# Optimization experiments

Measured on AMD Instinct MI355X. Metric: run time of the kernel, lower is better.

Reference implementation:

```python
import jax, jax.numpy as jnp
import numpy as np

D = 1024
H = 8
K = 6
TEMP = 0.1
LN_EPS = 1e-5


def _ln(x, g, b):
    m = jnp.mean(x, axis=-1, keepdims=True)
    v = jnp.mean((x - m) ** 2, axis=-1, keepdims=True)
    return (x - m) / jnp.sqrt(v + LN_EPS) * g + b


def setup_inputs() -> dict:
    key = jax.random.key(0)
    ks = jax.random.split(key, 8)
    B, T = 8, 4096
    s = 0.02
    inp = {
        'video_features': jax.random.normal(ks[0], (B, T, D), jnp.float32),
        'query_embedding': jax.random.normal(ks[1], (B, D), jnp.float32),
        'mu_w1': jax.random.normal(ks[2], (D, D), jnp.float32) * s,
        'mu_b1': jnp.zeros((D,), jnp.float32),
        'mu_g': jnp.ones((D,), jnp.float32),
        'mu_be': jnp.zeros((D,), jnp.float32),
        'mu_w2': jax.random.normal(ks[3], (D, D), jnp.float32) * s,
        'mu_b2': jnp.zeros((D,), jnp.float32),
        'sg_w1': jax.random.normal(ks[4], (D, D), jnp.float32) * s,
        'sg_b1': jnp.zeros((D,), jnp.float32),
        'sg_g': jnp.ones((D,), jnp.float32),
        'sg_be': jnp.zeros((D,), jnp.float32),
        'sg_w2': jax.random.normal(ks[5], (D, D), jnp.float32) * s,
        'sg_b2': jnp.zeros((D,), jnp.float32),
        'in_w': jax.random.normal(ks[6], (3 * D, D), jnp.float32) * s,
        'in_b': jnp.zeros((3 * D,), jnp.float32),
        'out_w': jax.random.normal(ks[7], (D, D), jnp.float32) * s,
        'out_b': jnp.zeros((D,), jnp.float32),
    }
    return inp


def reference(video_features, query_embedding, mu_w1, mu_b1, mu_g, mu_be, mu_w2, mu_b2,
              sg_w1, sg_b1, sg_g, sg_be, sg_w2, sg_b2, in_w, in_b, out_w, out_b):
    B, T, _ = video_features.shape
    dh = D // H

    # mu / sigma estimators (Linear -> LN -> ReLU -> Linear [-> Softplus])
    mu_q = jax.nn.relu(_ln(query_embedding @ mu_w1.T + mu_b1, mu_g, mu_be)) @ mu_w2.T + mu_b2  # [B,D]
    sigma_q = jax.nn.softplus(
        jax.nn.relu(_ln(query_embedding @ sg_w1.T + sg_b1, sg_g, sg_be)) @ sg_w2.T + sg_b2) + 1e-6

    # Mahalanobis (diagonal) distances [B,T]
    centered = video_features - mu_q[:, None, :]
    dist = jnp.sum(centered ** 2 / sigma_q[:, None, :], axis=-1)

    # distance weights around the (torch lower) median
    med = jnp.sort(dist, axis=1)[:, (T - 1) // 2][:, None]
    dist_w = jnp.exp(-jnp.abs(dist - med) / TEMP)  # [B,T]

    # single-query multihead attention (torch MHA, averaged attn weights)
    wq, wk, wv = in_w[:D], in_w[D:2 * D], in_w[2 * D:]
    bq, bk, bv = in_b[:D], in_b[D:2 * D], in_b[2 * D:]
    q = (mu_q @ wq.T + bq).reshape(B, H, dh)                  # [B,H,dh]
    k = (video_features @ wk.T + bk).reshape(B, T, H, dh)     # [B,T,H,dh]
    scores = jnp.einsum('bhd,bthd->bht', q, k) / jnp.sqrt(jnp.asarray(dh, q.dtype))
    attn = jax.nn.softmax(scores, axis=-1)                    # [B,H,T]
    attn_w = jnp.mean(attn, axis=1)                           # [B,T] head-averaged

    combined = dist_w * attn_w  # [B,T]

    # greedy diverse top-k (farthest-point style), vectorized over batch
    ar = jnp.arange(T)
    idx0 = jnp.argmax(combined, axis=1)                       # [B]
    sel_mask = ar[None, :] == idx0[:, None]
    min_d = jnp.abs(ar[None, :] - idx0[:, None]).astype(combined.dtype)
    picks = [idx0]
    for _ in range(K - 1):
        score = jnp.where(sel_mask, -jnp.inf, min_d * combined)
        nxt = jnp.argmax(score, axis=1)
        picks.append(nxt)
        sel_mask = sel_mask | (ar[None, :] == nxt[:, None])
        min_d = jnp.minimum(min_d, jnp.abs(ar[None, :] - nxt[:, None]).astype(combined.dtype))
    indices = jnp.stack(picks, axis=1)  # [B,K]

    rep = jnp.take_along_axis(video_features, indices[:, :, None], axis=1)  # [B,K,D]

    # NTLBG loss
    rep_dist = jnp.take_along_axis(dist, indices, axis=1)  # [B,K]
    target = jnp.sort(rep_dist, axis=1)[:, (K - 1) // 2][:, None]
    ellipsoid = jnp.mean((rep_dist - target) ** 2)
    centered_rep = rep - mu_q[:, None, :]
    consistency = jnp.mean(jnp.sum(centered_rep ** 2 / sigma_q[:, None, :], axis=-1))
    sim = jnp.einsum('bkd,bjd->bkj', rep, rep)
    tri = jnp.triu(jnp.ones((K, K), rep.dtype), k=1)
    diversity = jnp.mean((sim * tri) ** 2)
    loss = ellipsoid + 0.1 * consistency + 0.05 * diversity

    return rep, indices, combined, dist, mu_q, sigma_q, loss
```

## Files before the change

kernel.cpp:

```cpp
#include <hip/hip_runtime.h>
#include <math.h>

#define BD   8
#define TT   4096
#define DD   1024
#define HH   8
#define KK   6
#define OFF_REP   0
#define OFF_IDX   49152
#define OFF_COMB  49200
#define OFF_DIST  81968
#define OFF_MU    114736
#define OFF_SG    122928
#define OFF_LOSS  131120
#define WS_X1     0
#define WS_H      16384
#define WS_Q      32768
#define WS_P      40960
#define WS_C      106496
#define WS_ISIG   106560
#define WS_SCORES 114752

#define INV_SQRT_DH 0.08838834764831845f

__device__ __forceinline__ float softplus_f(float x) {
  return fmaxf(x, 0.0f) + log1pf(expf(-fabsf(x)));
}

__device__ __forceinline__ void gemv_rows_core(const float* __restrict__ in,
                                               const float* __restrict__ W,
                                               int row, float (*s_in)[DD], float acc[8]) {
  int tid = threadIdx.x;
  const float4* in4 = (const float4*)in;
  float4* s4 = (float4*)&s_in[0][0];
  for (int i = tid; i < 2048; i += 256) s4[i] = in4[i];
  __syncthreads();
  int lane = tid & 63;
  const float4* wr4 = (const float4*)(W + (size_t)row * DD);
#pragma unroll
  for (int b = 0; b < 8; ++b) acc[b] = 0.0f;
#pragma unroll
  for (int i = 0; i < 4; ++i) {
    int d4 = i * 64 + lane;
    float4 w4 = wr4[d4];
#pragma unroll
    for (int b = 0; b < 8; ++b) {
      float4 q4 = ((const float4*)&s_in[b][0])[d4];
      acc[b] += w4.x * q4.x + w4.y * q4.y + w4.z * q4.z + w4.w * q4.w;
    }
  }
#pragma unroll
  for (int off = 32; off; off >>= 1)
#pragma unroll
    for (int b = 0; b < 8; ++b) acc[b] += __shfl_xor(acc[b], off, 64);
}

__global__ __launch_bounds__(256) void k_gemv_pre(const float* __restrict__ qe,
    const float* __restrict__ W0, const float* __restrict__ W1,
    const float* __restrict__ b0, const float* __restrict__ b1, float* __restrict__ x1) {
  __shared__ float s_in[8][DD];
  int path = blockIdx.x >> 8;
  int row = (blockIdx.x & 255) * 4 + (threadIdx.x >> 6);
  const float* W = path ? W1 : W0;
  const float* bb = path ? b1 : b0;
  float acc[8];
  gemv_rows_core(qe, W, row, s_in, acc);
  if ((threadIdx.x & 63) == 0) {
    float bv = bb[row];
#pragma unroll
    for (int b = 0; b < 8; ++b) x1[path * 8192 + b * DD + row] = acc[b] + bv;
  }
}

__global__ __launch_bounds__(256) void k_ln(const float* __restrict__ x1,
    const float* __restrict__ g0, const float* __restrict__ be0,
    const float* __restrict__ g1, const float* __restrict__ be1, float* __restrict__ h) {
  int path = blockIdx.x >> 3, b = blockIdx.x & 7;
  const float* x = x1 + path * 8192 + b * DD;
  const float* g = path ? g1 : g0;
  const float* be = path ? be1 : be0;
  __shared__ float sx[DD];
  __shared__ float red[256];
  int tid = threadIdx.x;
  float ps = 0.0f;
  for (int i = tid; i < DD; i += 256) { float v = x[i]; sx[i] = v; ps += v; }
  red[tid] = ps; __syncthreads();
  for (int off = 128; off; off >>= 1) { if (tid < off) red[tid] += red[tid + off]; __syncthreads(); }
  float mean = red[0] * (1.0f / 1024.0f);
  __syncthreads();
  float pv = 0.0f;
  for (int i = tid; i < DD; i += 256) { float d = sx[i] - mean; pv += d * d; }
  red[tid] = pv; __syncthreads();
  for (int off = 128; off; off >>= 1) { if (tid < off) red[tid] += red[tid + off]; __syncthreads(); }
  float var = red[0] * (1.0f / 1024.0f);
  float inv = 1.0f / sqrtf(var + 1e-5f);
  for (int i = tid; i < DD; i += 256) {
    float v = (sx[i] - mean) * inv * g[i] + be[i];
    h[path * 8192 + b * DD + i] = v > 0.0f ? v : 0.0f;
  }
}

__global__ __launch_bounds__(256) void k_gemv_mid(const float* __restrict__ h,
    const float* __restrict__ W0, const float* __restrict__ W1,
    const float* __restrict__ b0, const float* __restrict__ b1,
    float* __restrict__ mu_out, float* __restrict__ sg_out, float* __restrict__ isig) {
  __shared__ float s_in[8][DD];
  int path = blockIdx.x >> 8;
  int row = (blockIdx.x & 255) * 4 + (threadIdx.x >> 6);
  const float* W = path ? W1 : W0;
  const float* bb = path ? b1 : b0;
  float acc[8];
  gemv_rows_core(h + path * 8192, W, row, s_in, acc);
  if ((threadIdx.x & 63) == 0) {
    float bv = bb[row];
#pragma unroll
    for (int b = 0; b < 8; ++b) {
      float v = acc[b] + bv;
      if (path == 0) {
        mu_out[b * DD + row] = v;
      } else {
        float sp = softplus_f(v) + 1e-6f;
        sg_out[b * DD + row] = sp;
        isig[b * DD + row] = 1.0f / sp;
      }
    }
  }
}

__global__ __launch_bounds__(256) void k_gemv_q(const float* __restrict__ mu_q,
    const float* __restrict__ in_w, const float* __restrict__ in_b, float* __restrict__ q) {
  __shared__ float s_in[8][DD];
  int row = blockIdx.x * 4 + (threadIdx.x >> 6);
  float acc[8];
  gemv_rows_core(mu_q, in_w, row, s_in, acc);
  if ((threadIdx.x & 63) == 0) {
    float bv = in_b[row];
#pragma unroll
    for (int b = 0; b < 8; ++b) q[b * DD + row] = acc[b] + bv;
  }
}

__global__ __launch_bounds__(256) void k_p(const float* __restrict__ q,
    const float* __restrict__ in_w, const float* __restrict__ in_b,
    float* __restrict__ p, float* __restrict__ c) {
  int hh = blockIdx.x >> 2;
  int j0 = (blockIdx.x & 3) * 256;
  __shared__ float qh[8][128];
  for (int i = threadIdx.x; i < 1024; i += 256) {
    int b = i >> 7, r = i & 127;
    qh[b][r] = q[b * DD + hh * 128 + r];
  }
  __syncthreads();
  const float* wbase = in_w + (size_t)(DD + hh * 128) * DD + j0 + threadIdx.x;
  float acc[8];
#pragma unroll
  for (int b = 0; b < 8; ++b) acc[b] = 0.0f;
  for (int r = 0; r < 128; ++r) {
    float w = wbase[(size_t)r * DD];
#pragma unroll
    for (int b = 0; b < 8; ++b) acc[b] += qh[b][r] * w;
  }
#pragma unroll
  for (int b = 0; b < 8; ++b) p[(b * HH + hh) * DD + j0 + threadIdx.x] = acc[b] * INV_SQRT_DH;
  if ((blockIdx.x & 3) == 0 && threadIdx.x < 8) {
    int b = threadIdx.x;
    float cc = 0.0f;
    for (int r = 0; r < 128; ++r) cc += qh[b][r] * in_b[DD + hh * 128 + r];
    c[b * HH + hh] = cc * INV_SQRT_DH;
  }
}

__global__ __launch_bounds__(256, 4) void k_main(const float* __restrict__ video,
    const float* __restrict__ mu_q, const float* __restrict__ isig,
    const float* __restrict__ p, const float* __restrict__ c,
    float* __restrict__ dist_out, float* __restrict__ scores, float* __restrict__ loss_out) {
  __shared__ float s_mu[DD];
  __shared__ float s_is[DD];
  __shared__ float s_p[HH][DD];
  int b = blockIdx.x >> 8;
  int chunk = blockIdx.x & 255;
  int tid = threadIdx.x;
  int wave = tid >> 6, lane = tid & 63;
  if (blockIdx.x == 0 && tid == 0) loss_out[0] = 0.0f;
  float4* s_mu4 = (float4*)s_mu;
  float4* s_is4 = (float4*)s_is;
  float4* s_p4 = (float4*)&s_p[0][0];
  s_mu4[tid] = ((const float4*)(mu_q + b * DD))[tid];
  s_is4[tid] = ((const float4*)(isig + b * DD))[tid];
  const float4* pg4 = (const float4*)(p + b * HH * DD);
  for (int i = tid; i < 2048; i += 256) s_p4[i] = pg4[i];
  __syncthreads();

  int t0 = chunk * 16 + wave * 4;
  const float4* v4 = (const float4*)(video + ((size_t)(b * TT + t0)) * DD);
  double dacc[4] = {0.0, 0.0, 0.0, 0.0};
  float sacc[4][8];
#pragma unroll
  for (int t = 0; t < 4; ++t)
#pragma unroll
    for (int hh = 0; hh < 8; ++hh) sacc[t][hh] = 0.0f;

#pragma unroll 2
  for (int i = 0; i < 4; ++i) {
    int d4 = i * 64 + lane;
    float4 vv0 = v4[0 * 256 + d4];
    float4 vv1 = v4[1 * 256 + d4];
    float4 vv2 = v4[2 * 256 + d4];
    float4 vv3 = v4[3 * 256 + d4];
    {
      float4 mu4 = s_mu4[d4];
      float4 is4 = s_is4[d4];
      float dx, dy, dz, dw, e;
      dx = vv0.x - mu4.x; dy = vv0.y - mu4.y; dz = vv0.z - mu4.z; dw = vv0.w - mu4.w;
      e = dx * dx * is4.x + dy * dy * is4.y + dz * dz * is4.z + dw * dw * is4.w;
      dacc[0] += (double)e;
      dx = vv1.x - mu4.x; dy = vv1.y - mu4.y; dz = vv1.z - mu4.z; dw = vv1.w - mu4.w;
      e = dx * dx * is4.x + dy * dy * is4.y + dz * dz * is4.z + dw * dw * is4.w;
      dacc[1] += (double)e;
      dx = vv2.x - mu4.x; dy = vv2.y - mu4.y; dz = vv2.z - mu4.z; dw = vv2.w - mu4.w;
      e = dx * dx * is4.x + dy * dy * is4.y + dz * dz * is4.z + dw * dw * is4.w;
      dacc[2] += (double)e;
      dx = vv3.x - mu4.x; dy = vv3.y - mu4.y; dz = vv3.z - mu4.z; dw = vv3.w - mu4.w;
      e = dx * dx * is4.x + dy * dy * is4.y + dz * dz * is4.z + dw * dw * is4.w;
      dacc[3] += (double)e;
    }
#pragma unroll
    for (int hh = 0; hh < 8; ++hh) {
      float4 pp = ((const float4*)&s_p[hh][0])[d4];
      sacc[0][hh] += pp.x * vv0.x + pp.y * vv0.y + pp.z * vv0.z + pp.w * vv0.w;
      sacc[1][hh] += pp.x * vv1.x + pp.y * vv1.y + pp.z * vv1.z + pp.w * vv1.w;
      sacc[2][hh] += pp.x * vv2.x + pp.y * vv2.y + pp.z * vv2.z + pp.w * vv2.w;
      sacc[3][hh] += pp.x * vv3.x + pp.y * vv3.y + pp.z * vv3.z + pp.w * vv3.w;
    }
  }
#pragma unroll
  for (int off = 32; off; off >>= 1) {
#pragma unroll
    for (int t = 0; t < 4; ++t) {
      dacc[t] += __shfl_xor(dacc[t], off, 64);
#pragma unroll
      for (int hh = 0; hh < 8; ++hh) sacc[t][hh] += __shfl_xor(sacc[t][hh], off, 64);
    }
  }
  if (lane < 4) {
    int t = lane;
    int tt = t0 + t;
    dist_out[b * TT + tt] = (float)dacc[t];
#pragma unroll
    for (int hh = 0; hh < 8; ++hh)
      scores[(size_t)(b * HH + hh) * TT + tt] = sacc[t][hh] + c[b * HH + hh];
  }
}

__global__ __launch_bounds__(1024) void k_epilogue(const float* __restrict__ scores,
    const float* __restrict__ dist, const float* __restrict__ video,
    float* __restrict__ comb_out, float* __restrict__ idx_out,
    float* __restrict__ rep, float* __restrict__ loss_out) {
  int b = blockIdx.x;
  int tid = threadIdx.x;
  int wave = tid >> 6, lane = tid & 63;
  __shared__ float s_dist[TT];
  __shared__ float s_hm[HH], s_hs[HH];
  __shared__ float s_w16[16], s_w16b[16];
  __shared__ unsigned hist[256];
  __shared__ unsigned wsum[4];
  __shared__ unsigned s_sel;
  __shared__ int s_kk;
  __shared__ float wv[16];
  __shared__ int wi[16];
  __shared__ int s_pick;
  __shared__ float wdiv[16];
  __shared__ float repb[KK * DD];

  {
    int h = tid >> 7, lt = tid & 127;
    const float4* srow4 = (const float4*)(scores + ((size_t)(b * HH + h)) * TT);
    float m = -INFINITY;
#pragma unroll
    for (int i = 0; i < 8; ++i) {
      float4 v = srow4[lt + i * 128];
      m = fmaxf(m, fmaxf(fmaxf(v.x, v.y), fmaxf(v.z, v.w)));
    }
#pragma unroll
    for (int off = 32; off; off >>= 1) m = fmaxf(m, __shfl_xor(m, off, 64));
    if (lane == 0) s_w16[wave] = m;
    __syncthreads();
    float mh = fmaxf(s_w16[h * 2], s_w16[h * 2 + 1]);
    float s = 0.0f;
#pragma unroll
    for (int i = 0; i < 8; ++i) {
      float4 v = srow4[lt + i * 128];
      s += expf(v.x - mh) + expf(v.y - mh) + expf(v.z - mh) + expf(v.w - mh);
    }
#pragma unroll
    for (int off = 32; off; off >>= 1) s += __shfl_xor(s, off, 64);
    if (lane == 0) s_w16b[wave] = s;
    __syncthreads();
    if (lt == 0) { s_hm[h] = mh; s_hs[h] = 1.0f / (s_w16b[h * 2] + s_w16b[h * 2 + 1]); }
    __syncthreads();
  }

  float4 d4 = ((const float4*)(dist + b * TT))[tid];
  ((float4*)s_dist)[tid] = d4;
  float4 aw = make_float4(0.f, 0.f, 0.f, 0.f);
#pragma unroll
  for (int h = 0; h < HH; ++h) {
    float4 sc = ((const float4*)(scores + ((size_t)(b * HH + h)) * TT))[tid];
    float mh = s_hm[h], is = s_hs[h];
    aw.x += expf(sc.x - mh) * is;
    aw.y += expf(sc.y - mh) * is;
    aw.z += expf(sc.z - mh) * is;
    aw.w += expf(sc.w - mh) * is;
  }
  aw.x *= 0.125f; aw.y *= 0.125f; aw.z *= 0.125f; aw.w *= 0.125f;
  uint4 keys;
  keys.x = __float_as_uint(d4.x);
  keys.y = __float_as_uint(d4.y);
  keys.z = __float_as_uint(d4.z);
  keys.w = __float_as_uint(d4.w);
  __syncthreads();

  unsigned prefix = 0;
  int kk = (TT - 1) / 2;
  for (int pass = 0; pass < 4; ++pass) {
    int shift = 24 - 8 * pass;
    if (tid < 256) hist[tid] = 0;
    __syncthreads();
    {
      unsigned karr[4] = {keys.x, keys.y, keys.z, keys.w};
#pragma unroll
      for (int j = 0; j < 4; ++j) {
        unsigned key = karr[j];
        bool ok = (pass == 0) || ((key >> (shift + 8)) == prefix);
        if (ok) atomicAdd(&hist[(key >> shift) & 255], 1u);
      }
    }
    __syncthreads();
    unsigned hcnt = 0, inc = 0;
    if (tid < 256) {
      hcnt = hist[tid];
      inc = hcnt;
#pragma unroll
      for (int off = 1; off < 64; off <<= 1) {
        unsigned v = __shfl_up(inc, off, 64);
        if (lane >= off) inc += v;
      }
      if (lane == 63) wsum[wave] = inc;
    }
    __syncthreads();
    if (tid < 256) {
      unsigned base = 0;
      for (int w = 0; w < wave; ++w) base += wsum[w];
      unsigned excl = base + inc - hcnt;
      if ((int)excl <= kk && kk < (int)(excl + hcnt)) {
        s_sel = (prefix << 8) | (unsigned)tid;
        s_kk = kk - (int)excl;
      }
    }
    __syncthreads();
    prefix = s_sel;
    kk = s_kk;
    __syncthreads();
  }
  float med = __uint_as_float(prefix);

  float4 cb;
  cb.x = expf(-fabsf(d4.x - med) / 0.1f) * aw.x;
  cb.y = expf(-fabsf(d4.y - med) / 0.1f) * aw.y;
  cb.z = expf(-fabsf(d4.z - med) / 0.1f) * aw.z;
  cb.w = expf(-fabsf(d4.w - med) / 0.1f) * aw.w;
  ((float4*)(comb_out + b * TT))[tid] = cb;

  float4 md = make_float4(0.f, 0.f, 0.f, 0.f);
  int i0 = tid * 4;
  int picks[KK];
  for (int k = 0; k < KK; ++k) {
    float carr[4] = {cb.x, cb.y, cb.z, cb.w};
    float marr[4] = {md.x, md.y, md.z, md.w};
    float best = -INFINITY; int bi = 1 << 30;
#pragma unroll
    for (int j = 0; j < 4; ++j) {
      float cv = carr[j];
      float sc = (k == 0) ? cv : ((cv < 0.0f) ? -INFINITY : marr[j] * cv);
      if (sc > best) { best = sc; bi = i0 + j; }
    }
#pragma unroll
    for (int off = 32; off; off >>= 1) {
      float ov = __shfl_xor(best, off, 64);
      int oi = __shfl_xor(bi, off, 64);
      if (ov > best || (ov == best && oi < bi)) { best = ov; bi = oi; }
    }
    if (lane == 0) { wv[wave] = best; wi[wave] = bi; }
    __syncthreads();
    if (tid == 0) {
      float bb2 = wv[0]; int ii = wi[0];
#pragma unroll
      for (int w = 1; w < 16; ++w)
        if (wv[w] > bb2 || (wv[w] == bb2 && wi[w] < ii)) { bb2 = wv[w]; ii = wi[w]; }
      s_pick = ii;
    }
    __syncthreads();
    int pick = s_pick;
    picks[k] = pick;
    if ((pick >> 2) == tid) {
      int j = pick & 3;
      if (j == 0) cb.x = -1.0f; else if (j == 1) cb.y = -1.0f;
      else if (j == 2) cb.z = -1.0f; else cb.w = -1.0f;
    }
    float dn0 = fabsf((float)(i0 + 0 - pick));
    float dn1 = fabsf((float)(i0 + 1 - pick));
    float dn2 = fabsf((float)(i0 + 2 - pick));
    float dn3 = fabsf((float)(i0 + 3 - pick));
    if (k == 0) { md.x = dn0; md.y = dn1; md.z = dn2; md.w = dn3; }
    else { md.x = fminf(md.x, dn0); md.y = fminf(md.y, dn1);
           md.z = fminf(md.z, dn2); md.w = fminf(md.w, dn3); }
  }
  if (tid < KK) idx_out[b * KK + tid] = (float)picks[tid];

  float4* repb4 = (float4*)repb;
  float4* rep4 = (float4*)(rep + (size_t)b * KK * DD);
  for (int e = tid; e < KK * (DD / 4); e += 1024) {
    int k = e >> 8, dd4 = e & 255;
    const float4* vrow = (const float4*)(video + ((size_t)(b * TT + picks[k])) * DD);
    float4 v = vrow[dd4];
    rep4[(size_t)k * (DD / 4) + dd4] = v;
    repb4[e] = v;
  }
  __syncthreads();

  const int pk[15] = {0,0,0,0,0,1,1,1,1,2,2,2,3,3,4};
  const int pj[15] = {1,2,3,4,5,2,3,4,5,3,4,5,4,5,5};
  float divacc = 0.0f;
  if (wave < 15) {
    int a = pk[wave], j = pj[wave];
    float part = 0.0f;
    for (int d = lane; d < DD; d += 64) part += repb[a * DD + d] * repb[j * DD + d];
#pragma unroll
    for (int off = 32; off; off >>= 1) part += __shfl_xor(part, off, 64);
    if (lane == 0) divacc = part * part;
  }
  if (lane == 0) wdiv[wave] = (wave < 15) ? divacc : 0.0f;
  __syncthreads();

  if (tid == 0) {
    float div = 0.0f;
#pragma unroll
    for (int w = 0; w < 15; ++w) div += wdiv[w];
    float rd[KK], srt[KK];
#pragma unroll
    for (int k = 0; k < KK; ++k) { rd[k] = s_dist[picks[k]]; srt[k] = rd[k]; }
    for (int a = 1; a < KK; ++a) {
      float key = srt[a]; int b2 = a - 1;
      while (b2 >= 0 && srt[b2] > key) { srt[b2 + 1] = srt[b2]; --b2; }
      srt[b2 + 1] = key;
    }
    float target = srt[(KK - 1) / 2];
    float ell = 0.0f, cons = 0.0f;
#pragma unroll
    for (int k = 0; k < KK; ++k) { float d = rd[k] - target; ell += d * d; cons += rd[k]; }
    float partial = ell * (1.0f / 48.0f) + 0.1f * cons * (1.0f / 48.0f) + 0.05f * div * (1.0f / 288.0f);
    atomicAdd(loss_out, partial);
  }
}

extern "C" void kernel_launch(void* const* d_in, const int* in_sizes, int n_in,
                              void* d_out, int out_size, void* d_ws, size_t ws_size,
                              hipStream_t stream) {
  const float* video = (const float*)d_in[0];
  const float* qe    = (const float*)d_in[1];
  const float* mu_w1 = (const float*)d_in[2];
  const float* mu_b1 = (const float*)d_in[3];
  const float* mu_g  = (const float*)d_in[4];
  const float* mu_be = (const float*)d_in[5];
  const float* mu_w2 = (const float*)d_in[6];
  const float* mu_b2 = (const float*)d_in[7];
  const float* sg_w1 = (const float*)d_in[8];
  const float* sg_b1 = (const float*)d_in[9];
  const float* sg_g  = (const float*)d_in[10];
  const float* sg_be = (const float*)d_in[11];
  const float* sg_w2 = (const float*)d_in[12];
  const float* sg_b2 = (const float*)d_in[13];
  const float* in_w  = (const float*)d_in[14];
  const float* in_b  = (const float*)d_in[15];
  float* out = (float*)d_out;
  float* ws  = (float*)d_ws;

  k_gemv_pre<<<512, 256, 0, stream>>>(qe, mu_w1, sg_w1, mu_b1, sg_b1, ws + WS_X1);
  k_ln<<<16, 256, 0, stream>>>(ws + WS_X1, mu_g, mu_be, sg_g, sg_be, ws + WS_H);
  k_gemv_mid<<<512, 256, 0, stream>>>(ws + WS_H, mu_w2, sg_w2, mu_b2, sg_b2,
                                      out + OFF_MU, out + OFF_SG, ws + WS_ISIG);
  k_gemv_q<<<256, 256, 0, stream>>>(out + OFF_MU, in_w, in_b, ws + WS_Q);
  k_p<<<32, 256, 0, stream>>>(ws + WS_Q, in_w, in_b, ws + WS_P, ws + WS_C);
  k_main<<<2048, 256, 0, stream>>>(video, out + OFF_MU, ws + WS_ISIG, ws + WS_P, ws + WS_C,
                                   out + OFF_DIST, ws + WS_SCORES, out + OFF_LOSS);
  k_epilogue<<<8, 1024, 0, stream>>>(ws + WS_SCORES, out + OFF_DIST, video,
                                     out + OFF_COMB, out + OFF_IDX, out + OFF_REP, out + OFF_LOSS);
}
```

Baseline: 332.2 us.

## Fuse softmax exp and sums into main kernel, privatize radix histogram

The main kernel now exponentiates the attention scores without max subtraction and accumulates per-head sums with shared then global atomics. The epilogue therefore only normalises instead of running separate max and sum passes over the scores. The per-batch query-bias constant c is dropped, since it cancels in the softmax. LayerNorm is rewritten as a single-pass float4 kernel with wave shuffles, and the median radix select uses per-wave private histograms to reduce atomic contention. Risks: exp overflow without a max shift, nondeterministic atomic sums, and less accurate single-pass variance.

```diff
diff --git a/kernel.cpp b/kernel.cpp
--- a/kernel.cpp
+++ b/kernel.cpp
@@ -17,9 +17,9 @@
 #define WS_H      16384
 #define WS_Q      32768
 #define WS_P      40960
-#define WS_C      106496
+#define WS_SUMS   106496
 #define WS_ISIG   106560
-#define WS_SCORES 114752
+#define WS_ES     114752
 
 #define INV_SQRT_DH 0.08838834764831845f
 
@@ -76,28 +76,32 @@
     const float* __restrict__ g0, const float* __restrict__ be0,
     const float* __restrict__ g1, const float* __restrict__ be1, float* __restrict__ h) {
   int path = blockIdx.x >> 3, b = blockIdx.x & 7;
-  const float* x = x1 + path * 8192 + b * DD;
-  const float* g = path ? g1 : g0;
-  const float* be = path ? be1 : be0;
-  __shared__ float sx[DD];
-  __shared__ float red[256];
-  int tid = threadIdx.x;
-  float ps = 0.0f;
-  for (int i = tid; i < DD; i += 256) { float v = x[i]; sx[i] = v; ps += v; }
-  red[tid] = ps; __syncthreads();
-  for (int off = 128; off; off >>= 1) { if (tid < off) red[tid] += red[tid + off]; __syncthreads(); }
-  float mean = red[0] * (1.0f / 1024.0f);
-  __syncthreads();
-  float pv = 0.0f;
-  for (int i = tid; i < DD; i += 256) { float d = sx[i] - mean; pv += d * d; }
-  red[tid] = pv; __syncthreads();
-  for (int off = 128; off; off >>= 1) { if (tid < off) red[tid] += red[tid + off]; __syncthreads(); }
-  float var = red[0] * (1.0f / 1024.0f);
+  const float4* x4 = (const float4*)(x1 + path * 8192 + b * DD);
+  const float4* g4 = (const float4*)(path ? g1 : g0);
+  const float4* be4 = (const float4*)(path ? be1 : be0);
+  int tid = threadIdx.x, wave = tid >> 6, lane = tid & 63;
+  __shared__ float ws1[4], ws2[4];
+  float4 v = x4[tid];
+  float s = v.x + v.y + v.z + v.w;
+  float s2 = v.x * v.x + v.y * v.y + v.z * v.z + v.w * v.w;
+#pragma unroll
+  for (int off = 32; off; off >>= 1) {
+    s += __shfl_xor(s, off, 64);
+    s2 += __shfl_xor(s2, off, 64);
+  }
+  if (lane == 0) { ws1[wave] = s; ws2[wave] = s2; }
+  __syncthreads();
+  s = ws1[0] + ws1[1] + ws1[2] + ws1[3];
+  s2 = ws2[0] + ws2[1] + ws2[2] + ws2[3];
+  float mean = s * (1.0f / 1024.0f);
+  float var = s2 * (1.0f / 1024.0f) - mean * mean;
   float inv = 1.0f / sqrtf(var + 1e-5f);
-  for (int i = tid; i < DD; i += 256) {
-    float v = (sx[i] - mean) * inv * g[i] + be[i];
-    h[path * 8192 + b * DD + i] = v > 0.0f ? v : 0.0f;
-  }
+  float4 g = g4[tid], be = be4[tid], o;
+  o.x = fmaxf((v.x - mean) * inv * g.x + be.x, 0.0f);
+  o.y = fmaxf((v.y - mean) * inv * g.y + be.y, 0.0f);
+  o.z = fmaxf((v.z - mean) * inv * g.z + be.z, 0.0f);
+  o.w = fmaxf((v.w - mean) * inv * g.w + be.w, 0.0f);
+  ((float4*)(h + path * 8192 + b * DD))[tid] = o;
 }
 
 __global__ __launch_bounds__(256) void k_gemv_mid(const float* __restrict__ h,
@@ -141,8 +145,12 @@
 }
 
 __global__ __launch_bounds__(256) void k_p(const float* __restrict__ q,
-    const float* __restrict__ in_w, const float* __restrict__ in_b,
-    float* __restrict__ p, float* __restrict__ c) {
+    const float* __restrict__ in_w, float* __restrict__ p,
+    float* __restrict__ sums, float* __restrict__ loss_out) {
+  if (blockIdx.x == 0) {
+    if (threadIdx.x < 64) sums[threadIdx.x] = 0.0f;
+    else if (threadIdx.x == 64) loss_out[0] = 0.0f;
+  }
   int hh = blockIdx.x >> 2;
   int j0 = (blockIdx.x & 3) * 256;
   __shared__ float qh[8][128];
@@ -162,26 +170,20 @@
   }
 #pragma unroll
   for (int b = 0; b < 8; ++b) p[(b * HH + hh) * DD + j0 + threadIdx.x] = acc[b] * INV_SQRT_DH;
-  if ((blockIdx.x & 3) == 0 && threadIdx.x < 8) {
-    int b = threadIdx.x;
-    float cc = 0.0f;
-    for (int r = 0; r < 128; ++r) cc += qh[b][r] * in_b[DD + hh * 128 + r];
-    c[b * HH + hh] = cc * INV_SQRT_DH;
-  }
 }
 
 __global__ __launch_bounds__(256, 4) void k_main(const float* __restrict__ video,
     const float* __restrict__ mu_q, const float* __restrict__ isig,
-    const float* __restrict__ p, const float* __restrict__ c,
-    float* __restrict__ dist_out, float* __restrict__ scores, float* __restrict__ loss_out) {
+    const float* __restrict__ p,
+    float* __restrict__ dist_out, float* __restrict__ es, float* __restrict__ sums) {
   __shared__ float s_mu[DD];
   __shared__ float s_is[DD];
   __shared__ float s_p[HH][DD];
+  __shared__ float s_esum[HH];
   int b = blockIdx.x >> 8;
   int chunk = blockIdx.x & 255;
   int tid = threadIdx.x;
   int wave = tid >> 6, lane = tid & 63;
-  if (blockIdx.x == 0 && tid == 0) loss_out[0] = 0.0f;
   float4* s_mu4 = (float4*)s_mu;
   float4* s_is4 = (float4*)s_is;
   float4* s_p4 = (float4*)&s_p[0][0];
@@ -189,6 +191,7 @@
   s_is4[tid] = ((const float4*)(isig + b * DD))[tid];
   const float4* pg4 = (const float4*)(p + b * HH * DD);
   for (int i = tid; i < 2048; i += 256) s_p4[i] = pg4[i];
+  if (tid < HH) s_esum[tid] = 0.0f;
   __syncthreads();
 
   int t0 = chunk * 16 + wave * 4;
@@ -247,12 +250,18 @@
     int tt = t0 + t;
     dist_out[b * TT + tt] = (float)dacc[t];
 #pragma unroll
-    for (int hh = 0; hh < 8; ++hh)
-      scores[(size_t)(b * HH + hh) * TT + tt] = sacc[t][hh] + c[b * HH + hh];
-  }
-}
-
-__global__ __launch_bounds__(1024) void k_epilogue(const float* __restrict__ scores,
+    for (int hh = 0; hh < 8; ++hh) {
+      float ev = expf(sacc[t][hh]);
+      es[(size_t)(b * HH + hh) * TT + tt] = ev;
+      atomicAdd(&s_esum[hh], ev);
+    }
+  }
+  __syncthreads();
+  if (tid < HH) atomicAdd(&sums[b * HH + tid], s_esum[tid]);
+}
+
+__global__ __launch_bounds__(1024) void k_epilogue(const float* __restrict__ es,
+    const float* __restrict__ sums,
     const float* __restrict__ dist, const float* __restrict__ video,
     float* __restrict__ comb_out, float* __restrict__ idx_out,
     float* __restrict__ rep, float* __restrict__ loss_out) {
@@ -260,9 +269,8 @@
   int tid = threadIdx.x;
   int wave = tid >> 6, lane = tid & 63;
   __shared__ float s_dist[TT];
-  __shared__ float s_hm[HH], s_hs[HH];
-  __shared__ float s_w16[16], s_w16b[16];
-  __shared__ unsigned hist[256];
+  __shared__ float s_hs[HH];
+  __shared__ unsigned whist[16][256];
   __shared__ unsigned wsum[4];
   __shared__ unsigned s_sel;
   __shared__ int s_kk;
@@ -272,45 +280,20 @@
   __shared__ float wdiv[16];
   __shared__ float repb[KK * DD];
 
-  {
-    int h = tid >> 7, lt = tid & 127;
-    const float4* srow4 = (const float4*)(scores + ((size_t)(b * HH + h)) * TT);
-    float m = -INFINITY;
-#pragma unroll
-    for (int i = 0; i < 8; ++i) {
-      float4 v = srow4[lt + i * 128];
-      m = fmaxf(m, fmaxf(fmaxf(v.x, v.y), fmaxf(v.z, v.w)));
-    }
-#pragma unroll
-    for (int off = 32; off; off >>= 1) m = fmaxf(m, __shfl_xor(m, off, 64));
-    if (lane == 0) s_w16[wave] = m;
-    __syncthreads();
-    float mh = fmaxf(s_w16[h * 2], s_w16[h * 2 + 1]);
-    float s = 0.0f;
-#pragma unroll
-    for (int i = 0; i < 8; ++i) {
-      float4 v = srow4[lt + i * 128];
-      s += expf(v.x - mh) + expf(v.y - mh) + expf(v.z - mh) + expf(v.w - mh);
-    }
-#pragma unroll
-    for (int off = 32; off; off >>= 1) s += __shfl_xor(s, off, 64);
-    if (lane == 0) s_w16b[wave] = s;
-    __syncthreads();
-    if (lt == 0) { s_hm[h] = mh; s_hs[h] = 1.0f / (s_w16b[h * 2] + s_w16b[h * 2 + 1]); }
-    __syncthreads();
-  }
+  if (tid < HH) s_hs[tid] = 1.0f / sums[b * HH + tid];
+  __syncthreads();
 
   float4 d4 = ((const float4*)(dist + b * TT))[tid];
   ((float4*)s_dist)[tid] = d4;
   float4 aw = make_float4(0.f, 0.f, 0.f, 0.f);
 #pragma unroll
   for (int h = 0; h < HH; ++h) {
-    float4 sc = ((const float4*)(scores + ((size_t)(b * HH + h)) * TT))[tid];
-    float mh = s_hm[h], is = s_hs[h];
-    aw.x += expf(sc.x - mh) * is;
-    aw.y += expf(sc.y - mh) * is;
-    aw.z += expf(sc.z - mh) * is;
-    aw.w += expf(sc.w - mh) * is;
+    float4 e4 = ((const float4*)(es + ((size_t)(b * HH + h)) * TT))[tid];
+    float is = s_hs[h];
+    aw.x += e4.x * is;
+    aw.y += e4.y * is;
+    aw.z += e4.z * is;
+    aw.w += e4.w * is;
   }
   aw.x *= 0.125f; aw.y *= 0.125f; aw.z *= 0.125f; aw.w *= 0.125f;
   uint4 keys;
@@ -318,13 +301,12 @@
   keys.y = __float_as_uint(d4.y);
   keys.z = __float_as_uint(d4.z);
   keys.w = __float_as_uint(d4.w);
-  __syncthreads();
 
   unsigned prefix = 0;
   int kk = (TT - 1) / 2;
   for (int pass = 0; pass < 4; ++pass) {
     int shift = 24 - 8 * pass;
-    if (tid < 256) hist[tid] = 0;
+    ((uint4*)whist)[tid] = make_uint4(0u, 0u, 0u, 0u);
     __syncthreads();
     {
       unsigned karr[4] = {keys.x, keys.y, keys.z, keys.w};
@@ -332,13 +314,14 @@
       for (int j = 0; j < 4; ++j) {
         unsigned key = karr[j];
         bool ok = (pass == 0) || ((key >> (shift + 8)) == prefix);
-        if (ok) atomicAdd(&hist[(key >> shift) & 255], 1u);
+        if (ok) atomicAdd(&whist[wave][(key >> shift) & 255], 1u);
       }
     }
     __syncthreads();
     unsigned hcnt = 0, inc = 0;
     if (tid < 256) {
-      hcnt = hist[tid];
+#pragma unroll
+      for (int w = 0; w < 16; ++w) hcnt += whist[w][tid];
       inc = hcnt;
 #pragma unroll
       for (int off = 1; off < 64; off <<= 1) {
@@ -490,9 +473,9 @@
   k_gemv_mid<<<512, 256, 0, stream>>>(ws + WS_H, mu_w2, sg_w2, mu_b2, sg_b2,
                                       out + OFF_MU, out + OFF_SG, ws + WS_ISIG);
   k_gemv_q<<<256, 256, 0, stream>>>(out + OFF_MU, in_w, in_b, ws + WS_Q);
-  k_p<<<32, 256, 0, stream>>>(ws + WS_Q, in_w, in_b, ws + WS_P, ws + WS_C);
-  k_main<<<2048, 256, 0, stream>>>(video, out + OFF_MU, ws + WS_ISIG, ws + WS_P, ws + WS_C,
-                                   out + OFF_DIST, ws + WS_SCORES, out + OFF_LOSS);
-  k_epilogue<<<8, 1024, 0, stream>>>(ws + WS_SCORES, out + OFF_DIST, video,
+  k_p<<<32, 256, 0, stream>>>(ws + WS_Q, in_w, ws + WS_P, ws + WS_SUMS, out + OFF_LOSS);
+  k_main<<<2048, 256, 0, stream>>>(video, out + OFF_MU, ws + WS_ISIG, ws + WS_P,
+                                   out + OFF_DIST, ws + WS_ES, ws + WS_SUMS);
+  k_epilogue<<<8, 1024, 0, stream>>>(ws + WS_ES, ws + WS_SUMS, out + OFF_DIST, video,
                                      out + OFF_COMB, out + OFF_IDX, out + OFF_REP, out + OFF_LOSS);
 }
```

Result: no change. 328.3 us (-1.2%).
